# Kernel tuning notes

Hardware: AMD Instinct MI355X
Metric: run time of the kernel (lower is better)

## Reference

```python
import jax, jax.numpy as jnp
import numpy as np
from jax import lax

B, M, L = 4, 20, 200
IN_C, C1, C2 = 2048, 512, 256
CDIM, DC1, DC2, SDIM = 300, 512, 256, 1024
NEG = -1e15  # -INFINITY in source


def conv1d(x, w, b, pad):
    # x: [N, Cin, L], w: [Cout, Cin, K]
    y = lax.conv_general_dilated(x, w, (1,), ((pad, pad),),
                                 dimension_numbers=('NCH', 'OIH', 'NCH'))
    return y + b[None, :, None]


def maxpool2(x):
    return lax.reduce_window(x, -jnp.inf, lax.max, (1, 1, 2), (1, 1, 2), 'VALID')


def deconv1d(x, w, b):
    # torch ConvTranspose1d(k=4, s=2, p=1): conv with lhs_dilation=2, pad k-1-p=2,
    # kernel flipped and in/out swapped. w: [Cin, Cout, K]
    wt = jnp.flip(w, -1).transpose(1, 0, 2)  # [Cout, Cin, K]
    y = lax.conv_general_dilated(x, wt, (1,), ((2, 2),), lhs_dilation=(2,),
                                 dimension_numbers=('NCH', 'OIH', 'NCH'))
    return y + b[None, :, None]


def setup_inputs() -> dict:
    key = jax.random.key(0)
    ks = jax.random.split(key, 16)
    p = lambda k, sh, s=0.02: (jax.random.normal(k, sh, jnp.float32) * s)
    return dict(
        batch=jax.random.normal(ks[0], (B, M, L, IN_C), jnp.float32),
        seg_len=jax.random.randint(ks[1], (B, M), 1, L + 1, jnp.int32),
        concept1=jax.random.normal(ks[2], (B, CDIM), jnp.float32),
        concept2=jax.random.normal(ks[3], (B, CDIM), jnp.float32),
        w_conv1=p(ks[4], (C1, IN_C, 5)), b_conv1=jnp.zeros((C1,), jnp.float32),
        w_conv2=p(ks[5], (C2, C1, 5)), b_conv2=jnp.zeros((C2,), jnp.float32),
        w_ca1=p(ks[6], (C2, CDIM)), w_ca2=p(ks[7], (C2, C2)), w_ca3=p(ks[8], (1, C2)),
        w_dc1=p(ks[9], (3 * C2, DC1, 4)), b_dc1=jnp.zeros((DC1,), jnp.float32),
        w_dc2=p(ks[10], (DC1, DC2, 4)), b_dc2=jnp.zeros((DC2,), jnp.float32),
        w_sim1=p(ks[11], (SDIM, DC2)), w_sim2=p(ks[12], (SDIM, CDIM)),
        w_mlp=p(ks[13], (1, SDIM)), b_mlp=jnp.zeros((1,), jnp.float32),
    )


def reference(batch, seg_len, concept1, concept2,
              w_conv1, b_conv1, w_conv2, b_conv2,
              w_ca1, w_ca2, w_ca3,
              w_dc1, b_dc1, w_dc2, b_dc2,
              w_sim1, w_sim2, w_mlp, b_mlp):
    Bs, Ms, Ls = batch.shape[:3]
    Lq = Ls // 4
    x = batch.reshape(Bs * Ms, Ls, -1).transpose(0, 2, 1)        # [BM, IN_C, L]
    t1 = maxpool2(conv1d(x, w_conv1, b_conv1, 2))                # [BM, C1, L/2]
    t2 = maxpool2(conv1d(t1, w_conv2, b_conv2, 2)).transpose(0, 2, 1)  # [BM, L/4, C2]

    # vectorized ragged mask: k < ceil(seg_len/4)
    mask = (jnp.arange(Lq)[None, None, :] < ((seg_len + 3) // 4)[:, :, None])
    mask = mask.reshape(Bs * Ms, Lq)

    kproj = t2 @ w_ca2.T                                         # [BM, Lq, C2]

    def concept_att(concept):
        # additive attention; scores are identical across the query-frame dim,
        # so compute one row and broadcast the weighted sum.
        q = concept @ w_ca1.T                                    # [B, C2]
        qe = jnp.repeat(q, Ms, axis=0)                           # [BM, C2]
        s = jnp.tanh(qe[:, None, :] + kproj) @ w_ca3[0]          # [BM, Lq]
        s = jnp.where(mask, s, NEG)
        a = jax.nn.softmax(s, axis=-1)
        r = jnp.einsum('bk,bkc->bc', a, t2)                      # [BM, C2]
        return jnp.broadcast_to(r[:, None, :], t2.shape)         # [BM, Lq, C2]

    r1 = concept_att(concept1)
    r2 = concept_att(concept2)

    cat = jnp.concatenate([t2, r1, r2], axis=-1).transpose(0, 2, 1)  # [BM, 3C2, Lq]
    d = deconv1d(cat, w_dc1, b_dc1)                              # [BM, DC1, L/2]
    d = deconv1d(d, w_dc2, b_dc2).transpose(0, 2, 1)             # [BM, L, DC2]
    d = d.reshape(Bs, Ms * Ls, -1)

    sim1 = d @ w_sim1.T                                          # [B, M*L, SDIM]
    c1 = concept1 @ w_sim2.T                                     # [B, SDIM]
    c2 = concept2 @ w_sim2.T
    sc1 = jax.nn.sigmoid((c1[:, None, :] * sim1) @ w_mlp[0] + b_mlp[0])
    sc2 = jax.nn.sigmoid((c2[:, None, :] * sim1) @ w_mlp[0] + b_mlp[0])
    return sc1.reshape(Bs, Ms, Ls), sc2.reshape(Bs, Ms, Ls)
```

## Files before the change

kernel.cpp:

```cpp
#include <hip/hip_runtime.h>
#include <hip/hip_bf16.h>
#include <math.h>

#define BB 4
#define MM 20
#define LL 200
#define INC 2048
#define C1 512
#define C2 256
#define CDIM 300
#define DC1 512
#define DC2 256
#define SDIM 1024
#define BM 80
#define L2 100
#define L4 50

typedef unsigned short u16;
typedef __attribute__((ext_vector_type(8))) short bf16x8;
typedef __attribute__((ext_vector_type(4))) float f32x4;

__device__ __forceinline__ u16 f2bf_rne(float f) {
  unsigned u = __float_as_uint(f);
  unsigned r = u + 0x7FFFu + ((u >> 16) & 1u);
  return (u16)(r >> 16);
}
__device__ __forceinline__ float bf2f(u16 v) {
  return __uint_as_float(((unsigned)v) << 16);
}

__device__ __forceinline__ void gload16(const u16* g, u16* l) {
  __builtin_amdgcn_global_load_lds(
      (const __attribute__((address_space(1))) void*)g,
      (__attribute__((address_space(3))) void*)l, 16, 0, 0);
}

__global__ void k_cast_pad_batch(const float* __restrict__ in, u16* __restrict__ out) {
  int idx = blockIdx.x * 256 + threadIdx.x;
  if (idx >= 80 * 204 * 256) return;
  int c8 = idx % 256;
  int pi = (idx / 256) % 204;
  int n  = idx / (256 * 204);
  uint4 o = make_uint4(0u, 0u, 0u, 0u);
  if (pi >= 2 && pi < 202) {
    const float* p = in + ((long long)(n * 200 + pi - 2) * 2048 + c8 * 8);
    float4 a = *(const float4*)p;
    float4 b = *(const float4*)(p + 4);
    o.x = (unsigned)f2bf_rne(a.x) | ((unsigned)f2bf_rne(a.y) << 16);
    o.y = (unsigned)f2bf_rne(a.z) | ((unsigned)f2bf_rne(a.w) << 16);
    o.z = (unsigned)f2bf_rne(b.x) | ((unsigned)f2bf_rne(b.y) << 16);
    o.w = (unsigned)f2bf_rne(b.z) | ((unsigned)f2bf_rne(b.w) << 16);
  }
  *(uint4*)(out + (long long)idx * 8) = o;
}

__global__ void k_zero_pad(u16* __restrict__ p, int ncnt, int rpad, int lr, int P,
                           int cin8, int total) {
  int idx = blockIdx.x * 256 + threadIdx.x;
  if (idx >= total) return;
  int c = idx % cin8;
  int pr = (idx / cin8) % (rpad - lr);
  int n = idx / (cin8 * (rpad - lr));
  int row = (pr < P) ? pr : lr + pr;
  *(uint4*)(p + ((long long)(n * rpad + row) * cin8 + c) * 8) = make_uint4(0, 0, 0, 0);
}

__global__ void k_cast_bf16(const float* __restrict__ in, u16* __restrict__ out, int n8) {
  int idx = blockIdx.x * 256 + threadIdx.x;
  if (idx >= n8) return;
  const float4* p = (const float4*)in + (long long)idx * 2;
  float4 a = p[0], b = p[1];
  uint4 o;
  o.x = (unsigned)f2bf_rne(a.x) | ((unsigned)f2bf_rne(a.y) << 16);
  o.y = (unsigned)f2bf_rne(a.z) | ((unsigned)f2bf_rne(a.w) << 16);
  o.z = (unsigned)f2bf_rne(b.x) | ((unsigned)f2bf_rne(b.y) << 16);
  o.w = (unsigned)f2bf_rne(b.z) | ((unsigned)f2bf_rne(b.w) << 16);
  *(uint4*)(out + (long long)idx * 8) = o;
}

__global__ void k_conv_w_t(const float* __restrict__ in, u16* __restrict__ out,
                           int Cout, int Cin, int Kk) {
  int idx = blockIdx.x * 256 + threadIdx.x;
  int total = Cout * Cin * Kk;
  if (idx >= total) return;
  int ci = idx % Cin;
  int t  = (idx / Cin) % Kk;
  int co = idx / (Cin * Kk);
  out[idx] = f2bf_rne(in[(co * Cin + ci) * Kk + t]);
}

__global__ void k_deconv_w_par(const float* __restrict__ in, u16* __restrict__ out,
                               int Cin, int Cout) {
  int idx = blockIdx.x * 256 + threadIdx.x;
  int total = Cin * Cout * 4;
  if (idx >= total) return;
  int ci = idx % Cin;
  int tt = (idx / Cin) & 1;
  int co = (idx / (2 * Cin)) % Cout;
  int zz = idx / (2 * Cin * Cout);
  out[idx] = f2bf_rne(in[(ci * Cout + co) * 4 + 3 - zz - 2 * tt]);
}

__global__ __launch_bounds__(256) void k_prep_small(
    const float* __restrict__ concept1, const float* __restrict__ concept2,
    const float* __restrict__ w_ca1, const float* __restrict__ w_sim1,
    const float* __restrict__ w_sim2, const float* __restrict__ w_mlp,
    float* __restrict__ qv) {
  int cz = blockIdx.x >> 2;
  int b  = blockIdx.x & 3;
  const float* con = cz ? concept2 : concept1;
  __shared__ float cvec[CDIM];
  __shared__ float chat[SDIM];
  int tid = threadIdx.x;
  for (int j = tid; j < CDIM; j += 256) cvec[j] = con[b * CDIM + j];
  __syncthreads();
  float accq = 0.f;
  for (int j = 0; j < CDIM; ++j) accq += cvec[j] * w_ca1[tid * CDIM + j];
  qv[(cz * 4 + b) * 256 + tid] = accq;
  for (int i = 0; i < 4; ++i) {
    int s = tid + i * 256;
    float a2 = 0.f;
    for (int j = 0; j < CDIM; ++j) a2 += cvec[j] * w_sim2[s * CDIM + j];
    chat[s] = a2 * w_mlp[s];
  }
  __syncthreads();
  float v = 0.f;
  for (int s = 0; s < SDIM; ++s) v += w_sim1[s * 256 + tid] * chat[s];
  qv[2048 + (cz * 4 + b) * 256 + tid] = v;
}

#define EP_PLAIN 0
#define EP_POOL  1
#define EP_ILV   2

template <int EP>
__global__ __launch_bounds__(256) void k_gemm(
    const u16* __restrict__ A, const u16* __restrict__ Bw,
    void* __restrict__ Co, const float* __restrict__ bias,
    int M, int N, int Ktot, int nchunk,
    int lr, int rpad, int cin, int off0c,
    int gx, int gy, long long sB, int orpad, int ooff) {
  __shared__ __align__(16) u16 As[2][8192];
  __shared__ __align__(16) u16 Bs[2][8192];
  int id = blockIdx.x;
  int x = (id >> 3) % gx;
  int y = (id & 7) + 8 * ((id >> 3) / gx);
  if (y >= gy) return;
  int z = blockIdx.z;
  int off0 = (EP == EP_ILV) ? z : off0c;
  int row0 = y * 128, col0 = x * 128;
  int tid = threadIdx.x, w = tid >> 6, ln = tid & 63;
  const u16* Bz = Bw + (long long)z * sB;

  const u16* ga[4];
  const u16* gb[4];
  #pragma unroll
  for (int i = 0; i < 4; ++i) {
    int f = 4 * w + i, blk = f >> 1, ks = f & 1;
    int klocal = ks * 32 + (ln >> 4) * 8;
    int ar = row0 + blk * 16 + (ln & 15);
    int n_ = ar / lr, l_ = ar - n_ * lr;
    ga[i] = A + ((long long)(n_ * rpad + l_ + off0) * cin + klocal);
    int br = col0 + blk * 16 + (ln & 15);
    gb[i] = Bz + ((long long)br * Ktot + klocal);
  }
  int wbase = 4 * w * 512;

  f32x4 acc[4][4];
  #pragma unroll
  for (int i = 0; i < 4; ++i)
    #pragma unroll
    for (int j = 0; j < 4; ++j) acc[i][j] = (f32x4){0.f, 0.f, 0.f, 0.f};

  int wr2 = (w >> 1) * 4;
  int wc2 = (w & 1) * 4;

  #pragma unroll
  for (int i = 0; i < 4; ++i) {
    gload16(ga[i], As[0] + wbase + i * 512);
    gload16(gb[i], Bs[0] + wbase + i * 512);
    ga[i] += 64;
    gb[i] += 64;
  }
  __syncthreads();

  for (int c = 0; c < nchunk; ++c) {
    int cur = c & 1;
    if (c + 1 < nchunk) {
      u16* dA = As[cur ^ 1] + wbase;
      u16* dB = Bs[cur ^ 1] + wbase;
      #pragma unroll
      for (int i = 0; i < 4; ++i) {
        gload16(ga[i], dA + i * 512);
        gload16(gb[i], dB + i * 512);
        ga[i] += 64;
        gb[i] += 64;
      }
    }
    #pragma unroll
    for (int ks = 0; ks < 2; ++ks) {
      bf16x8 af[4], bf[4];
      #pragma unroll
      for (int mi = 0; mi < 4; ++mi)
        af[mi] = *(const bf16x8*)&As[cur][(((wr2 + mi) * 2 + ks) * 512) + ln * 8];
      #pragma unroll
      for (int ni = 0; ni < 4; ++ni)
        bf[ni] = *(const bf16x8*)&Bs[cur][(((wc2 + ni) * 2 + ks) * 512) + ln * 8];
      #pragma unroll
      for (int mi = 0; mi < 4; ++mi)
        #pragma unroll
        for (int ni = 0; ni < 4; ++ni)
          acc[mi][ni] = __builtin_amdgcn_mfma_f32_16x16x32_bf16(
              af[mi], bf[ni], acc[mi][ni], 0, 0, 0);
    }
    __syncthreads();
  }

  int c15 = ln & 15, q4 = (ln >> 4) * 4;
  int wrow = (w >> 1) * 64, wcol = (w & 1) * 64;
  if (EP == EP_PLAIN) {
    float* Cz = (float*)Co;
    #pragma unroll
    for (int mi = 0; mi < 4; ++mi) {
      int gbase = row0 + wrow + mi * 16 + q4;
      #pragma unroll
      for (int r = 0; r < 4; ++r) {
        int grow = gbase + r;
        if (grow < M) {
          #pragma unroll
          for (int ni = 0; ni < 4; ++ni) {
            int col = col0 + wcol + ni * 16 + c15;
            Cz[(long long)grow * N + col] = acc[mi][ni][r];
          }
        }
      }
    }
  } else if (EP == EP_POOL) {
    u16* Cz = (u16*)Co;
    int lrh = lr >> 1;
    #pragma unroll
    for (int mi = 0; mi < 4; ++mi) {
      int gbase = row0 + wrow + mi * 16 + q4;
      #pragma unroll
      for (int p = 0; p < 2; ++p) {
        int grow = gbase + 2 * p;
        if (grow < M) {
          int prow = grow >> 1;
          int n = prow / lrh, ll = prow - n * lrh;
          long long orow = (long long)n * orpad + ooff + ll;
          #pragma unroll
          for (int ni = 0; ni < 4; ++ni) {
            int col = col0 + wcol + ni * 16 + c15;
            float v = fmaxf(acc[mi][ni][2 * p], acc[mi][ni][2 * p + 1]) + bias[col];
            Cz[orow * N + col] = f2bf_rne(v);
          }
        }
      }
    }
  } else {
    u16* Cz = (u16*)Co;
    #pragma unroll
    for (int mi = 0; mi < 4; ++mi) {
      int gbase = row0 + wrow + mi * 16 + q4;
      #pragma unroll
      for (int r = 0; r < 4; ++r) {
        int grow = gbase + r;
        if (grow < M) {
          int n = grow / lr, l = grow - n * lr;
          long long orow = (long long)n * orpad + ooff + 2 * l + z;
          #pragma unroll
          for (int ni = 0; ni < 4; ++ni) {
            int col = col0 + wcol + ni * 16 + c15;
            Cz[orow * N + col] = f2bf_rne(acc[mi][ni][r] + bias[col]);
          }
        }
      }
    }
  }
}

__global__ __launch_bounds__(256) void k_attention(
    const float* __restrict__ kproj, const u16* __restrict__ t2b,
    const float* __restrict__ qv, const float* __restrict__ w_ca3,
    const int* __restrict__ seg_len, u16* __restrict__ rb) {
  int bm = blockIdx.x % BM;
  int cz = blockIdx.x / BM;
  int b = bm / MM;
  int tid = threadIdx.x, w = tid >> 6, ln = tid & 63;
  __shared__ float sq[256], sw[256], sa[L4 + 14];
  sq[tid] = qv[(cz * 4 + b) * 256 + tid];
  sw[tid] = w_ca3[tid];
  __syncthreads();
  int kmax = (seg_len[bm] + 3) >> 2;
  for (int k = w; k < L4; k += 4) {
    float val = 0.f;
    #pragma unroll
    for (int i = 0; i < 4; ++i) {
      int c = ln + 64 * i;
      val += tanhf(sq[c] + kproj[(bm * L4 + k) * 256 + c]) * sw[c];
    }
    for (int off = 32; off > 0; off >>= 1) val += __shfl_down(val, off, 64);
    if (ln == 0) sa[k] = (k < kmax) ? val : -1e15f;
  }
  __syncthreads();
  if (w == 0) {
    float sv = (ln < L4) ? sa[ln] : -3e38f;
    float mx = sv;
    for (int off = 32; off > 0; off >>= 1) mx = fmaxf(mx, __shfl_down(mx, off, 64));
    mx = __shfl(mx, 0, 64);
    float e = (ln < L4) ? expf(sv - mx) : 0.f;
    float s = e;
    for (int off = 32; off > 0; off >>= 1) s += __shfl_down(s, off, 64);
    s = __shfl(s, 0, 64);
    if (ln < L4) sa[ln] = e / s;
  }
  __syncthreads();
  float r = 0.f;
  for (int k = 0; k < L4; ++k) r += sa[k] * bf2f(t2b[(bm * L4 + k) * 256 + tid]);
  rb[(cz * BM + bm) * 256 + tid] = f2bf_rne(r);
}

__global__ void k_build_cat(const u16* __restrict__ t2b, const u16* __restrict__ rb,
                            u16* __restrict__ catm, int total) {
  int idx = blockIdx.x * 256 + threadIdx.x;
  if (idx >= total) return;
  int ci = idx % 768;
  int row = idx / 768;
  int bm = row / L4, li = row - bm * L4;
  u16 v;
  if (ci < 256)      v = t2b[row * 256 + ci];
  else if (ci < 512) v = rb[bm * 256 + (ci - 256)];
  else               v = rb[(BM + bm) * 256 + (ci - 512)];
  catm[((long long)(bm * 52 + 1 + li)) * 768 + ci] = v;
}

__global__ __launch_bounds__(256) void k_final(
    const u16* __restrict__ d2b, const float* __restrict__ qv,
    const float* __restrict__ b_mlp, float* __restrict__ out) {
  int row = blockIdx.x;
  int n = row / LL, lo = row % LL;
  int b = n / MM, m = n % MM;
  int tid = threadIdx.x;
  float v = bf2f(d2b[(long long)row * 256 + tid]);
  float p1 = v * qv[2048 + (0 * 4 + b) * 256 + tid];
  float p2 = v * qv[2048 + (1 * 4 + b) * 256 + tid];
  for (int off = 32; off > 0; off >>= 1) {
    p1 += __shfl_down(p1, off, 64);
    p2 += __shfl_down(p2, off, 64);
  }
  __shared__ float s1[4], s2[4];
  if ((tid & 63) == 0) { s1[tid >> 6] = p1; s2[tid >> 6] = p2; }
  __syncthreads();
  if (tid == 0) {
    float bmlp = b_mlp[0];
    float a1 = s1[0] + s1[1] + s1[2] + s1[3] + bmlp;
    float a2 = s2[0] + s2[1] + s2[2] + s2[3] + bmlp;
    int t_idx = m * LL + lo;
    out[b * 4000 + t_idx]         = 1.f / (1.f + expf(-a1));
    out[16000 + b * 4000 + t_idx] = 1.f / (1.f + expf(-a2));
  }
}

extern "C" void kernel_launch(void* const* d_in, const int* in_sizes, int n_in,
                              void* d_out, int out_size, void* d_ws, size_t ws_size,
                              hipStream_t stream) {
  const float* batch    = (const float*)d_in[0];
  const int*   seg_len  = (const int*)d_in[1];
  const float* concept1 = (const float*)d_in[2];
  const float* concept2 = (const float*)d_in[3];
  const float* w_conv1  = (const float*)d_in[4];
  const float* b_conv1  = (const float*)d_in[5];
  const float* w_conv2  = (const float*)d_in[6];
  const float* b_conv2  = (const float*)d_in[7];
  const float* w_ca1    = (const float*)d_in[8];
  const float* w_ca2    = (const float*)d_in[9];
  const float* w_ca3    = (const float*)d_in[10];
  const float* w_dc1    = (const float*)d_in[11];
  const float* b_dc1    = (const float*)d_in[12];
  const float* w_dc2    = (const float*)d_in[13];
  const float* b_dc2    = (const float*)d_in[14];
  const float* w_sim1   = (const float*)d_in[15];
  const float* w_sim2   = (const float*)d_in[16];
  const float* w_mlp    = (const float*)d_in[17];
  const float* b_mlp    = (const float*)d_in[18];
  float* out = (float*)d_out;

  float* ws = (float*)d_ws;
  const long long off_qv    = 0;
  const long long off_kproj = 4096;
  const long long off_rb    = 1028096;
  const long long off_t1    = 1048576;
  const long long off_t2    = 3211264;
  const long long off_w1b   = 3735552;
  const long long off_w2b   = 6356992;
  const long long off_wd1p  = 6684672;
  const long long off_wd2p  = 7471104;
  const long long off_wca2b = 7733248;
  const long long off_BIG   = 7766016;

  u16* rb    = (u16*)(ws + off_rb);
  u16* t1b   = (u16*)(ws + off_t1);
  u16* t2b   = (u16*)(ws + off_t2);
  u16* w1b   = (u16*)(ws + off_w1b);
  u16* w2b   = (u16*)(ws + off_w2b);
  u16* wd1p  = (u16*)(ws + off_wd1p);
  u16* wd2p  = (u16*)(ws + off_wd2p);
  u16* wca2b = (u16*)(ws + off_wca2b);
  u16* batchb = (u16*)(ws + off_BIG);
  u16* catm   = (u16*)(ws + off_BIG);
  u16* d1b    = (u16*)(ws + off_BIG) + 3342336;
  u16* d2b    = (u16*)(ws + off_BIG) + 7667712;

  k_cast_pad_batch<<<dim3(16320), 256, 0, stream>>>(batch, batchb);
  k_conv_w_t<<<dim3(20480), 256, 0, stream>>>(w_conv1, w1b, C1, INC, 5);
  k_conv_w_t<<<dim3(2560), 256, 0, stream>>>(w_conv2, w2b, C2, C1, 5);
  k_deconv_w_par<<<dim3(6144), 256, 0, stream>>>(w_dc1, wd1p, 3 * C2, DC1);
  k_deconv_w_par<<<dim3(2048), 256, 0, stream>>>(w_dc2, wd2p, DC1, DC2);
  k_cast_bf16<<<dim3(32), 256, 0, stream>>>(w_ca2, wca2b, 8192);
  k_prep_small<<<dim3(8), 256, 0, stream>>>(concept1, concept2, w_ca1, w_sim1, w_sim2,
                                            w_mlp, ws + off_qv);
  k_zero_pad<<<dim3(80), 256, 0, stream>>>(t1b, 80, 104, 100, 2, 64, 20480);

  k_gemm<EP_POOL><<<dim3(512), 256, 0, stream>>>(
      batchb, w1b, t1b, b_conv1, 16000, 512, 10240, 160,
      200, 204, 2048, 0, 4, 125, 0, 104, 2);

  k_zero_pad<<<dim3(60), 256, 0, stream>>>(catm, 80, 52, 50, 1, 96, 15360);
  k_zero_pad<<<dim3(40), 256, 0, stream>>>(d1b, 80, 102, 100, 1, 64, 10240);

  k_gemm<EP_POOL><<<dim3(128), 256, 0, stream>>>(
      t1b, w2b, t2b, b_conv2, 8000, 256, 2560, 40,
      100, 104, 512, 0, 2, 63, 0, 50, 0);

  k_gemm<EP_PLAIN><<<dim3(64), 256, 0, stream>>>(
      t2b, wca2b, ws + off_kproj, nullptr, 4000, 256, 256, 4,
      4000, 4000, 256, 0, 2, 32, 0, 0, 0);

  k_attention<<<dim3(160), 256, 0, stream>>>(ws + off_kproj, t2b, ws + off_qv,
                                             w_ca3, seg_len, rb);

  k_build_cat<<<dim3(12000), 256, 0, stream>>>(t2b, rb, catm, 4000 * 768);

  k_gemm<EP_ILV><<<dim3(128, 1, 2), 256, 0, stream>>>(
      catm, wd1p, d1b, b_dc1, 4000, 512, 1536, 24,
      50, 52, 768, 0, 4, 32, 786432LL, 102, 1);

  k_gemm<EP_ILV><<<dim3(128, 1, 2), 256, 0, stream>>>(
      d1b, wd2p, d2b, b_dc2, 8000, 256, 1024, 16,
      100, 102, 512, 0, 2, 63, 262144LL, 200, 0);

  k_final<<<dim3(16000), 256, 0, stream>>>(d2b, ws + off_qv, b_mlp, out);
}
```

Baseline: 872.8 us.

## Reorder GEMM K-loop tap-major, refine waitcnt barriers, and remap block tiling

The conv and deconv GEMMs now walk the K dimension tap by tap within each 64-channel slice. Both pointers step by cin and wrap back afterwards, so neighbouring K chunks read overlapping input rows and can hit in cache instead of streaming fresh data. The main loop replaces the two __syncthreads with an explicit vmcnt wait plus raw s_barrier and sched_barrier. This lets the prefetch of the next chunk stay in flight while the current chunk is computed. Block-to-tile mapping also changes to a configurable px/yspan grouping, and the first GEMM grid shrinks to 504 blocks. The risks are that the hand-set vmcnt count is fragile, and that every call's argument list has to match the new K traversal order.

```diff
diff --git a/kernel.cpp b/kernel.cpp
--- a/kernel.cpp
+++ b/kernel.cpp
@@ -138,13 +138,14 @@
     const u16* __restrict__ A, const u16* __restrict__ Bw,
     void* __restrict__ Co, const float* __restrict__ bias,
     int M, int N, int Ktot, int nchunk,
-    int lr, int rpad, int cin, int off0c,
-    int gx, int gy, long long sB, int orpad, int ooff) {
+    int lr, int rpad, int cin, int off0c, int taps,
+    int px, int yspan, int gy, long long sB, int orpad, int ooff) {
   __shared__ __align__(16) u16 As[2][8192];
   __shared__ __align__(16) u16 Bs[2][8192];
   int id = blockIdx.x;
-  int x = (id >> 3) % gx;
-  int y = (id & 7) + 8 * ((id >> 3) / gx);
+  int k8 = id & 7, j = id >> 3;
+  int x = k8 / px, h = k8 - x * px;
+  int y = h * yspan + j;
   if (y >= gy) return;
   int z = blockIdx.z;
   int off0 = (EP == EP_ILV) ? z : off0c;
@@ -170,19 +171,26 @@
   #pragma unroll
   for (int i = 0; i < 4; ++i)
     #pragma unroll
-    for (int j = 0; j < 4; ++j) acc[i][j] = (f32x4){0.f, 0.f, 0.f, 0.f};
+    for (int j2 = 0; j2 < 4; ++j2) acc[i][j2] = (f32x4){0.f, 0.f, 0.f, 0.f};
 
   int wr2 = (w >> 1) * 4;
   int wc2 = (w & 1) * 4;
+
+  long long dstep = cin;
+  long long dwrap = 64 - (long long)(taps - 1) * cin;
+  int tc = 0;
 
   #pragma unroll
   for (int i = 0; i < 4; ++i) {
     gload16(ga[i], As[0] + wbase + i * 512);
     gload16(gb[i], Bs[0] + wbase + i * 512);
-    ga[i] += 64;
-    gb[i] += 64;
-  }
-  __syncthreads();
+  }
+  {
+    long long d = (tc == taps - 1) ? dwrap : dstep;
+    tc = (tc == taps - 1) ? 0 : tc + 1;
+    #pragma unroll
+    for (int i = 0; i < 4; ++i) { ga[i] += d; gb[i] += d; }
+  }
 
   for (int c = 0; c < nchunk; ++c) {
     int cur = c & 1;
@@ -193,10 +201,17 @@
       for (int i = 0; i < 4; ++i) {
         gload16(ga[i], dA + i * 512);
         gload16(gb[i], dB + i * 512);
-        ga[i] += 64;
-        gb[i] += 64;
       }
-    }
+      long long d = (tc == taps - 1) ? dwrap : dstep;
+      tc = (tc == taps - 1) ? 0 : tc + 1;
+      #pragma unroll
+      for (int i = 0; i < 4; ++i) { ga[i] += d; gb[i] += d; }
+      asm volatile("s_waitcnt vmcnt(8)" ::: "memory");
+    } else {
+      asm volatile("s_waitcnt vmcnt(0)" ::: "memory");
+    }
+    __builtin_amdgcn_s_barrier();
+    __builtin_amdgcn_sched_barrier(0);
     #pragma unroll
     for (int ks = 0; ks < 2; ++ks) {
       bf16x8 af[4], bf[4];
@@ -213,7 +228,8 @@
           acc[mi][ni] = __builtin_amdgcn_mfma_f32_16x16x32_bf16(
               af[mi], bf[ni], acc[mi][ni], 0, 0, 0);
     }
-    __syncthreads();
+    __builtin_amdgcn_sched_barrier(0);
+    __builtin_amdgcn_s_barrier();
   }
 
   int c15 = ln & 15, q4 = (ln >> 4) * 4;
@@ -421,20 +437,20 @@
                                             w_mlp, ws + off_qv);
   k_zero_pad<<<dim3(80), 256, 0, stream>>>(t1b, 80, 104, 100, 2, 64, 20480);
 
-  k_gemm<EP_POOL><<<dim3(512), 256, 0, stream>>>(
+  k_gemm<EP_POOL><<<dim3(504), 256, 0, stream>>>(
       batchb, w1b, t1b, b_conv1, 16000, 512, 10240, 160,
-      200, 204, 2048, 0, 4, 125, 0, 104, 2);
+      200, 204, 2048, 0, 5, 2, 63, 125, 0, 104, 2);
 
   k_zero_pad<<<dim3(60), 256, 0, stream>>>(catm, 80, 52, 50, 1, 96, 15360);
   k_zero_pad<<<dim3(40), 256, 0, stream>>>(d1b, 80, 102, 100, 1, 64, 10240);
 
   k_gemm<EP_POOL><<<dim3(128), 256, 0, stream>>>(
       t1b, w2b, t2b, b_conv2, 8000, 256, 2560, 40,
-      100, 104, 512, 0, 2, 63, 0, 50, 0);
+      100, 104, 512, 0, 5, 4, 16, 63, 0, 50, 0);
 
   k_gemm<EP_PLAIN><<<dim3(64), 256, 0, stream>>>(
       t2b, wca2b, ws + off_kproj, nullptr, 4000, 256, 256, 4,
-      4000, 4000, 256, 0, 2, 32, 0, 0, 0);
+      4000, 4000, 256, 0, 1, 4, 8, 32, 0, 0, 0);
 
   k_attention<<<dim3(160), 256, 0, stream>>>(ws + off_kproj, t2b, ws + off_qv,
                                              w_ca3, seg_len, rb);
@@ -443,11 +459,11 @@
 
   k_gemm<EP_ILV><<<dim3(128, 1, 2), 256, 0, stream>>>(
       catm, wd1p, d1b, b_dc1, 4000, 512, 1536, 24,
-      50, 52, 768, 0, 4, 32, 786432LL, 102, 1);
+      50, 52, 768, 0, 2, 2, 16, 32, 786432LL, 102, 1);
 
   k_gemm<EP_ILV><<<dim3(128, 1, 2), 256, 0, stream>>>(
       d1b, wd2p, d2b, b_dc2, 8000, 256, 1024, 16,
-      100, 102, 512, 0, 2, 63, 262144LL, 200, 0);
+      100, 102, 512, 0, 2, 4, 16, 63, 262144LL, 200, 0);
 
   k_final<<<dim3(16000), 256, 0, stream>>>(d2b, ws + off_qv, b_mlp, out);
 }
```

Result: no change. 874.5 us (+0.2%).
